# Kernel optimization log

Hardware: AMD Instinct MI355X
Metric: run time of the kernel (lower is better)

The kernel has to match this reference:

```python
import jax, jax.numpy as jnp
import numpy as np

N, M, D = 8192, 8192, 64


def _ball_points(key, n, d, r_lo=0.1, r_hi=0.85):
    k1, k2 = jax.random.split(key)
    v = jax.random.normal(k1, (n, d), dtype=jnp.float32)
    v = v / jnp.linalg.norm(v, axis=1, keepdims=True)
    r = jax.random.uniform(k2, (n, 1), dtype=jnp.float32, minval=r_lo, maxval=r_hi)
    return v * r  # points strictly inside the unit ball


def setup_inputs() -> dict:
    key = jax.random.key(0)
    ka, kb = jax.random.split(key)
    a = _ball_points(ka, N, D)
    b = _ball_points(kb, M, D)
    return {"a": a, "b": b}


def reference(a, b):
    # squared norms [N], [M]
    a2 = jnp.sum(a * a, axis=1)
    b2 = jnp.sum(b * b, axis=1)
    # pairwise Euclidean distance via GEMM trick: ||a||^2 + ||b||^2 - 2 a.b
    sq = a2[:, None] + b2[None, :] - 2.0 * (a @ b.T)  # [N, M]
    d = jnp.sqrt(jnp.maximum(sq, 0.0))
    # Poincare-style scaling (note: module uses distance d, not d^2)
    denom = (1.0 - a2)[:, None] * (1.0 - b2)[None, :]  # [N, M]
    inner = 1.0 + 2.0 * d / denom
    # arcosh(x) = log(x + sqrt(x^2 - 1))
    return jnp.log(inner + jnp.sqrt(inner * inner - 1.0))
```

## Files before the change

kernel.cpp:

```cpp
#include <hip/hip_runtime.h>

typedef unsigned short ushort_t;
typedef short bf16x8 __attribute__((ext_vector_type(8)));
typedef float f32x4 __attribute__((ext_vector_type(4)));

#define NPTS 8192
#define DIM 64

__global__ __launch_bounds__(256) void prep_kernel(
    const float* __restrict__ a, const float* __restrict__ b,
    ushort_t* __restrict__ ahi, ushort_t* __restrict__ alo,
    ushort_t* __restrict__ bhi, ushort_t* __restrict__ blo,
    float* __restrict__ a2, float* __restrict__ iva,
    float* __restrict__ b2, float* __restrict__ ivb)
{
    int which = blockIdx.x >> 11;
    int idx = (blockIdx.x & 2047) * 256 + threadIdx.x;
    const float* src = which ? b : a;
    ushort_t* hi = which ? bhi : ahi;
    ushort_t* lo = which ? blo : alo;
    float* s2 = which ? b2 : a2;
    float* iv = which ? ivb : iva;
    float scale = which ? 1.0f : 2.0f;

    float v = src[idx];
    unsigned u = __float_as_uint(v);
    unsigned hb = (u + 0x7fffu + ((u >> 16) & 1u)) >> 16;
    float hf = __uint_as_float(hb << 16);
    float l = v - hf;
    unsigned ul = __float_as_uint(l);
    unsigned lb = (ul + 0x7fffu + ((ul >> 16) & 1u)) >> 16;
    hi[idx] = (ushort_t)hb;
    lo[idx] = (ushort_t)lb;
    float p = v * v;
    #pragma unroll
    for (int m = 1; m < 64; m <<= 1) p += __shfl_xor(p, m, 64);
    if ((threadIdx.x & 63) == 0) {
        int row = idx >> 6;
        s2[row] = p;
        iv[row] = scale / (1.0f - p);
    }
}

__global__ __launch_bounds__(256, 4) void poincare_kernel(
    const ushort_t* __restrict__ ahi, const ushort_t* __restrict__ alo,
    const ushort_t* __restrict__ bhi, const ushort_t* __restrict__ blo,
    const float* __restrict__ a2v, const float* __restrict__ iva,
    const float* __restrict__ b2v, const float* __restrict__ ivb,
    float* __restrict__ out)
{
    int lane = threadIdx.x & 63;
    int wid  = threadIdx.x >> 6;
    int bx = blockIdx.x & 127;
    int by = blockIdx.x >> 7;
    int row0 = by * 128 + (wid >> 1) * 64;
    int col0 = bx * 64 + (wid & 1) * 32;
    int r16 = lane & 15;
    int kq  = lane >> 4;

    bf16x8 bfh[2][2], bfl[2][2];
    #pragma unroll
    for (int cb = 0; cb < 2; ++cb)
        #pragma unroll
        for (int ks = 0; ks < 2; ++ks) {
            int off = (col0 + cb * 16 + r16) * DIM + ks * 32 + kq * 8;
            bfh[cb][ks] = *(const bf16x8*)(bhi + off);
            bfl[cb][ks] = *(const bf16x8*)(blo + off);
        }

    f32x4 acc[4][2];
    #pragma unroll
    for (int rb = 0; rb < 4; ++rb)
        #pragma unroll
        for (int cb = 0; cb < 2; ++cb)
            acc[rb][cb] = (f32x4){0.f, 0.f, 0.f, 0.f};

    #pragma unroll
    for (int rb = 0; rb < 4; ++rb) {
        bf16x8 afh[2], afl[2];
        #pragma unroll
        for (int ks = 0; ks < 2; ++ks) {
            int off = (row0 + rb * 16 + r16) * DIM + ks * 32 + kq * 8;
            afh[ks] = *(const bf16x8*)(ahi + off);
            afl[ks] = *(const bf16x8*)(alo + off);
        }
        #pragma unroll
        for (int cb = 0; cb < 2; ++cb) {
            f32x4 c = acc[rb][cb];
            #pragma unroll
            for (int ks = 0; ks < 2; ++ks) {
                c = __builtin_amdgcn_mfma_f32_16x16x32_bf16(afh[ks], bfh[cb][ks], c, 0, 0, 0);
                c = __builtin_amdgcn_mfma_f32_16x16x32_bf16(afh[ks], bfl[cb][ks], c, 0, 0, 0);
                c = __builtin_amdgcn_mfma_f32_16x16x32_bf16(afl[ks], bfh[cb][ks], c, 0, 0, 0);
            }
            acc[rb][cb] = c;
        }
    }

    float b2c[2], ivc[2];
    #pragma unroll
    for (int cb = 0; cb < 2; ++cb) {
        int col = col0 + cb * 16 + r16;
        b2c[cb] = b2v[col];
        ivc[cb] = ivb[col];
    }

    #pragma unroll
    for (int rb = 0; rb < 4; ++rb) {
        #pragma unroll
        for (int r = 0; r < 4; ++r) {
            int row = row0 + rb * 16 + kq * 4 + r;
            float a2r = a2v[row];
            float ivr = iva[row];
            float* orow = out + (size_t)row * NPTS + col0;
            #pragma unroll
            for (int cb = 0; cb < 2; ++cb) {
                float dot = acc[rb][cb][r];
                float sq = fmaf(-2.0f, dot, a2r + b2c[cb]);
                sq = fmaxf(sq, 0.0f);
                float d = __builtin_amdgcn_sqrtf(sq);
                float inner = fmaf(d, ivr * ivc[cb], 1.0f);
                float t = fmaf(inner, inner, -1.0f);
                t = fmaxf(t, 0.0f);
                float st = __builtin_amdgcn_sqrtf(t);
                __builtin_nontemporal_store(__logf(inner + st), &orow[cb * 16 + r16]);
            }
        }
    }
}

extern "C" void kernel_launch(void* const* d_in, const int* in_sizes, int n_in,
                              void* d_out, int out_size, void* d_ws, size_t ws_size,
                              hipStream_t stream)
{
    const float* a = (const float*)d_in[0];
    const float* b = (const float*)d_in[1];
    float* out = (float*)d_out;
    char* ws = (char*)d_ws;

    ushort_t* ahi = (ushort_t*)(ws);
    ushort_t* alo = (ushort_t*)(ws + (1u << 20));
    ushort_t* bhi = (ushort_t*)(ws + (2u << 20));
    ushort_t* blo = (ushort_t*)(ws + (3u << 20));
    float* a2v = (float*)(ws + (4u << 20));
    float* iva = (float*)(ws + (4u << 20) + 32768);
    float* b2v = (float*)(ws + (4u << 20) + 65536);
    float* ivb = (float*)(ws + (4u << 20) + 98304);

    prep_kernel<<<4096, 256, 0, stream>>>(a, b, ahi, alo, bhi, blo,
                                          a2v, iva, b2v, ivb);
    poincare_kernel<<<128 * 64, 256, 0, stream>>>(
        ahi, alo, bhi, blo, a2v, iva, b2v, ivb, out);
}
```

Measured before the change: 332.1 us.

## Swap MFMA operands for row-contiguous 16-byte stores and enlarge tile to 128x128

Swaps the MFMA A/B operands so each lane's accumulator holds four consecutive columns of one row. This lets the epilogue write one 16-byte vector store per lane instead of scattered 4-byte nontemporal stores, and load b2/ivb as f32x4. The block tile grows from 128x64 to 128x128 to reuse the A fragments across more columns, which doubles the accumulator registers. The occupancy hint in launch_bounds is dropped, and the nontemporal store hint is lost.

```diff
diff --git a/kernel.cpp b/kernel.cpp
--- a/kernel.cpp
+++ b/kernel.cpp
@@ -42,7 +42,7 @@
     }
 }
 
-__global__ __launch_bounds__(256, 4) void poincare_kernel(
+__global__ __launch_bounds__(256) void poincare_kernel(
     const ushort_t* __restrict__ ahi, const ushort_t* __restrict__ alo,
     const ushort_t* __restrict__ bhi, const ushort_t* __restrict__ blo,
     const float* __restrict__ a2v, const float* __restrict__ iva,
@@ -51,80 +51,81 @@
 {
     int lane = threadIdx.x & 63;
     int wid  = threadIdx.x >> 6;
-    int bx = blockIdx.x & 127;
-    int by = blockIdx.x >> 7;
+    int bx = blockIdx.x & (NPTS / 128 - 1);
+    int by = blockIdx.x / (NPTS / 128);
     int row0 = by * 128 + (wid >> 1) * 64;
-    int col0 = bx * 64 + (wid & 1) * 32;
+    int col0 = bx * 128 + (wid & 1) * 64;
     int r16 = lane & 15;
     int kq  = lane >> 4;
 
-    bf16x8 bfh[2][2], bfl[2][2];
+    bf16x8 bfh[4][2], bfl[4][2];
     #pragma unroll
-    for (int cb = 0; cb < 2; ++cb)
+    for (int bc = 0; bc < 4; ++bc)
         #pragma unroll
         for (int ks = 0; ks < 2; ++ks) {
-            int off = (col0 + cb * 16 + r16) * DIM + ks * 32 + kq * 8;
-            bfh[cb][ks] = *(const bf16x8*)(bhi + off);
-            bfl[cb][ks] = *(const bf16x8*)(blo + off);
+            int off = (col0 + bc * 16 + r16) * DIM + ks * 32 + kq * 8;
+            bfh[bc][ks] = *(const bf16x8*)(bhi + off);
+            bfl[bc][ks] = *(const bf16x8*)(blo + off);
         }
 
-    f32x4 acc[4][2];
+    f32x4 acc[4][4];
     #pragma unroll
-    for (int rb = 0; rb < 4; ++rb)
+    for (int ar = 0; ar < 4; ++ar)
         #pragma unroll
-        for (int cb = 0; cb < 2; ++cb)
-            acc[rb][cb] = (f32x4){0.f, 0.f, 0.f, 0.f};
+        for (int bc = 0; bc < 4; ++bc)
+            acc[ar][bc] = (f32x4){0.f, 0.f, 0.f, 0.f};
 
     #pragma unroll
-    for (int rb = 0; rb < 4; ++rb) {
+    for (int ar = 0; ar < 4; ++ar) {
         bf16x8 afh[2], afl[2];
         #pragma unroll
         for (int ks = 0; ks < 2; ++ks) {
-            int off = (row0 + rb * 16 + r16) * DIM + ks * 32 + kq * 8;
+            int off = (row0 + ar * 16 + r16) * DIM + ks * 32 + kq * 8;
             afh[ks] = *(const bf16x8*)(ahi + off);
             afl[ks] = *(const bf16x8*)(alo + off);
         }
         #pragma unroll
-        for (int cb = 0; cb < 2; ++cb) {
-            f32x4 c = acc[rb][cb];
+        for (int bc = 0; bc < 4; ++bc) {
+            f32x4 c = acc[ar][bc];
             #pragma unroll
             for (int ks = 0; ks < 2; ++ks) {
-                c = __builtin_amdgcn_mfma_f32_16x16x32_bf16(afh[ks], bfh[cb][ks], c, 0, 0, 0);
-                c = __builtin_amdgcn_mfma_f32_16x16x32_bf16(afh[ks], bfl[cb][ks], c, 0, 0, 0);
-                c = __builtin_amdgcn_mfma_f32_16x16x32_bf16(afl[ks], bfh[cb][ks], c, 0, 0, 0);
+                c = __builtin_amdgcn_mfma_f32_16x16x32_bf16(bfh[bc][ks], afh[ks], c, 0, 0, 0);
+                c = __builtin_amdgcn_mfma_f32_16x16x32_bf16(bfl[bc][ks], afh[ks], c, 0, 0, 0);
+                c = __builtin_amdgcn_mfma_f32_16x16x32_bf16(bfh[bc][ks], afl[ks], c, 0, 0, 0);
             }
-            acc[rb][cb] = c;
+            acc[ar][bc] = c;
         }
     }
 
-    float b2c[2], ivc[2];
+    f32x4 b2c[4], ivc[4];
     #pragma unroll
-    for (int cb = 0; cb < 2; ++cb) {
-        int col = col0 + cb * 16 + r16;
-        b2c[cb] = b2v[col];
-        ivc[cb] = ivb[col];
+    for (int bc = 0; bc < 4; ++bc) {
+        b2c[bc] = *(const f32x4*)&b2v[col0 + bc * 16 + 4 * kq];
+        ivc[bc] = *(const f32x4*)&ivb[col0 + bc * 16 + 4 * kq];
     }
 
     #pragma unroll
-    for (int rb = 0; rb < 4; ++rb) {
+    for (int ar = 0; ar < 4; ++ar) {
+        int row = row0 + ar * 16 + r16;
+        float a2r = a2v[row];
+        float ivr = iva[row];
+        float* orow = out + (size_t)row * NPTS + col0;
         #pragma unroll
-        for (int r = 0; r < 4; ++r) {
-            int row = row0 + rb * 16 + kq * 4 + r;
-            float a2r = a2v[row];
-            float ivr = iva[row];
-            float* orow = out + (size_t)row * NPTS + col0;
+        for (int bc = 0; bc < 4; ++bc) {
+            f32x4 dots = acc[ar][bc];
+            f32x4 res;
             #pragma unroll
-            for (int cb = 0; cb < 2; ++cb) {
-                float dot = acc[rb][cb][r];
-                float sq = fmaf(-2.0f, dot, a2r + b2c[cb]);
+            for (int r = 0; r < 4; ++r) {
+                float sq = fmaf(-2.0f, dots[r], a2r + b2c[bc][r]);
                 sq = fmaxf(sq, 0.0f);
                 float d = __builtin_amdgcn_sqrtf(sq);
-                float inner = fmaf(d, ivr * ivc[cb], 1.0f);
+                float inner = fmaf(d, ivr * ivc[bc][r], 1.0f);
                 float t = fmaf(inner, inner, -1.0f);
                 t = fmaxf(t, 0.0f);
                 float st = __builtin_amdgcn_sqrtf(t);
-                __builtin_nontemporal_store(__logf(inner + st), &orow[cb * 16 + r16]);
+                res[r] = __logf(inner + st);
             }
+            *(f32x4*)&orow[bc * 16 + 4 * kq] = res;
         }
     }
 }
@@ -149,6 +150,6 @@
 
     prep_kernel<<<4096, 256, 0, stream>>>(a, b, ahi, alo, bhi, blo,
                                           a2v, iva, b2v, ivb);
-    poincare_kernel<<<128 * 64, 256, 0, stream>>>(
+    poincare_kernel<<<(NPTS / 128) * (NPTS / 128), 256, 0, stream>>>(
         ahi, alo, bhi, blo, a2v, iva, b2v, ivb, out);
 }
```

New measurement: 303.6 us. 8.6% less time.
